# Optimization experiments

Hardware: AMD Instinct MI355X
Metric: run time of the kernel (lower is better)

The kernel has to match this reference:

```python
import jax, jax.numpy as jnp
import numpy as np
import math

IN_DIM = 256
OUT_DIM = 256
H = 4
DK = OUT_DIM // H  # 64
N = 40000
E = 300000
T = 2  # node types
R = 3  # relations: 0:(A->B), 1:(B->A), 2:(A->B)


def setup_inputs() -> dict:
    key = jax.random.key(0)
    ks = jax.random.split(key, 24)
    def xavier(k, shape):
        fan_in, fan_out = shape[-2], shape[-1]
        lim = math.sqrt(6.0 / (fan_in + fan_out))
        return jax.random.uniform(k, shape, jnp.float32, -lim, lim)
    inp = {
        "hA": jax.random.normal(ks[0], (N, IN_DIM), jnp.float32),
        "hB": jax.random.normal(ks[1], (N, IN_DIM), jnp.float32),
        "src0": jax.random.randint(ks[2], (E,), 0, N, jnp.int32),
        "dst0": jax.random.randint(ks[3], (E,), 0, N, jnp.int32),
        "src1": jax.random.randint(ks[4], (E,), 0, N, jnp.int32),
        "dst1": jax.random.randint(ks[5], (E,), 0, N, jnp.int32),
        "src2": jax.random.randint(ks[6], (E,), 0, N, jnp.int32),
        "dst2": jax.random.randint(ks[7], (E,), 0, N, jnp.int32),
        # per-node-type linear weights, stacked [T, in, out]
        "Wk": xavier(ks[8], (T, IN_DIM, OUT_DIM)),
        "bk": jnp.zeros((T, OUT_DIM), jnp.float32),
        "Wq": xavier(ks[9], (T, IN_DIM, OUT_DIM)),
        "bq": jnp.zeros((T, OUT_DIM), jnp.float32),
        "Wv": xavier(ks[10], (T, IN_DIM, OUT_DIM)),
        "bv": jnp.zeros((T, OUT_DIM), jnp.float32),
        "Wa": xavier(ks[11], (T, OUT_DIM, OUT_DIM)),
        "ba": jnp.zeros((T, OUT_DIM), jnp.float32),
        "rel_att": xavier(ks[12], (R, H, DK, DK)),
        "rel_msg": xavier(ks[13], (R, H, DK, DK)),
        "rel_pri": jnp.ones((R, H), jnp.float32),
        "skip": jnp.ones((T,), jnp.float32),
    }
    return inp


def _hgt_forward(hA, hB, Wk, bk, Wq, bq, Wv, bv, Wa, ba,
                 rel_att, rel_msg, rel_pri, skip, edges):
    h = [hA, hB]
    sqrt_dk = math.sqrt(DK)

    def proj(W, b, x, t):
        return (x @ W[t] + b[t]).reshape(-1, H, DK)

    def rel_agg(r, s, d, src, dst):
        # relation-specific transforms
        k = jnp.einsum('nhi,hij->nhj', proj(Wk, bk, h[s], s), rel_att[r])
        v = jnp.einsum('nhi,hij->nhj', proj(Wv, bv, h[s], s), rel_msg[r])
        q = proj(Wq, bq, h[d], d)
        nd = h[d].shape[0]
        # per-edge dot-product attention score [E, H]
        score = jnp.einsum('ehd,ehd->eh', q[dst], k[src]) * rel_pri[r] / sqrt_dk
        # edge softmax normalized by destination node
        m = jax.ops.segment_max(score, dst, num_segments=nd)
        e = jnp.exp(score - m[dst])
        denom = jax.ops.segment_sum(e, dst, num_segments=nd)
        attn = e / denom[dst]
        # weighted scatter-sum aggregation -> [nd, H, DK]
        return jax.ops.segment_sum(v[src] * attn[:, :, None], dst, num_segments=nd)

    (src0, dst0), (src1, dst1), (src2, dst2) = edges
    agg0 = rel_agg(0, 0, 1, src0, dst0)  # A -> B
    agg1 = rel_agg(1, 1, 0, src1, dst1)  # B -> A
    agg2 = rel_agg(2, 0, 1, src2, dst2)  # A -> B

    # cross_reducer='mean' over etypes per destination type
    t_A = agg1.reshape(-1, OUT_DIM)
    t_B = ((agg0 + agg2) * 0.5).reshape(-1, OUT_DIM)

    def ts_aggr(t, n_id, h_dst):
        alpha = jax.nn.sigmoid(skip[n_id])
        trans = t @ Wa[n_id] + ba[n_id]  # dropout p=0.0 -> identity
        return trans * alpha + h_dst * (1.0 - alpha)

    out_A = ts_aggr(t_A, 0, hA)
    out_B = ts_aggr(t_B, 1, hB)
    return jnp.stack([out_A, out_B])  # [2, N, OUT_DIM]


def reference(hA, hB, src0, dst0, src1, dst1, src2, dst2,
              Wk, bk, Wq, bq, Wv, bv, Wa, ba,
              rel_att, rel_msg, rel_pri, skip):
    edges = ((src0, dst0), (src1, dst1), (src2, dst2))
    return _hgt_forward(hA, hB, Wk, bk, Wq, bq, Wv, bv, Wa, ba,
                        rel_att, rel_msg, rel_pri, skip, edges)
```

## Files before the change

kernel.cpp:

```cpp
#include <hip/hip_runtime.h>

#define NN 40000
#define EE 300000
#define DIM 256
#define NHD 4
#define CAP 64
#define LOG2E 1.4426950408889634f

typedef __attribute__((ext_vector_type(8))) short bfrag;
typedef __attribute__((ext_vector_type(4))) float fx4;

static __device__ __forceinline__ float bflo(unsigned u) {
  union { unsigned i; float f; } v; v.i = u << 16; return v.f;
}
static __device__ __forceinline__ float bfhi(unsigned u) {
  union { unsigned i; float f; } v; v.i = u & 0xffff0000u; return v.f;
}
static __device__ __forceinline__ unsigned short f2bf(float f) {
  union { float f; unsigned i; } v; v.f = f;
  unsigned x = v.i;
  return (unsigned short)((x + 0x7fffu + ((x >> 16) & 1u)) >> 16);
}
static __device__ __forceinline__ void gload_lds16(const unsigned short* g, unsigned short* l) {
  __builtin_amdgcn_global_load_lds((const __attribute__((address_space(1))) void*)g,
                                   (__attribute__((address_space(3))) void*)l, 16, 0, 0);
}

static __device__ __forceinline__ void map_rc(int L, int NC, int NR, int& rb, int& cb) {
  int per = 8 * NC;
  int g = L / per;
  int base = g * 8;
  int rig = NR - base; if (rig > 8) rig = 8;
  int idx = L - g * per;
  rb = base + idx % rig;
  cb = idx / rig;
}

static __device__ __forceinline__ void gemm_core64(const unsigned short* __restrict__ X,
                                                   const unsigned short* __restrict__ WT,
                                                   int R0, int C0,
                                                   fx4 acc[2][4],
                                                   unsigned short* ldsA,
                                                   unsigned short* ldsB) {
  const int tid = threadIdx.x;
  const int wave = tid >> 6, lane = tid & 63;
  const int li = lane & 15, lk = lane >> 4;
  const int wr = wave >> 1, wc = wave & 1;
  const int lr = lane >> 3;
  const int swz = ((lane & 7) ^ lr) * 8;
#pragma unroll
  for (int kt = 0; kt < 4; ++kt) {
    const int k0 = kt * 64;
    if (kt) __syncthreads();
#pragma unroll
    for (int i = 0; i < 6; ++i) {
      int g = wave * 6 + i;
      if (g < 8) gload_lds16(X + (size_t)(R0 + g * 8 + lr) * DIM + k0 + swz, ldsA + g * 512);
      else       gload_lds16(WT + (size_t)(C0 + (g - 8) * 8 + lr) * DIM + k0 + swz, ldsB + (g - 8) * 512);
    }
    __syncthreads();
#pragma unroll
    for (int ks = 0; ks < 2; ++ks) {
      bfrag a[2], b[4];
      const int chb = (lk + ks * 4) ^ (li & 7);
#pragma unroll
      for (int mt = 0; mt < 2; ++mt)
        a[mt] = *(const bfrag*)(ldsA + (wr * 32 + mt * 16 + li) * 64 + chb * 8);
#pragma unroll
      for (int nt = 0; nt < 4; ++nt)
        b[nt] = *(const bfrag*)(ldsB + (wc * 64 + nt * 16 + li) * 64 + chb * 8);
#pragma unroll
      for (int mt = 0; mt < 2; ++mt)
#pragma unroll
        for (int nt = 0; nt < 4; ++nt)
          acc[mt][nt] = __builtin_amdgcn_mfma_f32_16x16x32_bf16(a[mt], b[nt], acc[mt][nt], 0, 0, 0);
    }
  }
}

__global__ __launch_bounds__(256) void cvt_kernel(const float* __restrict__ hA,
                                                  const float* __restrict__ hB,
                                                  unsigned short* __restrict__ XA,
                                                  unsigned short* __restrict__ XB) {
  long id = (long)blockIdx.x * 256 + threadIdx.x;
  const long half = (long)NN * DIM / 8;
  const float4* src; unsigned short* dst; long o;
  if (id < half) { src = (const float4*)hA; dst = XA; o = id; }
  else           { src = (const float4*)hB; dst = XB; o = id - half; }
  float4 a = src[o * 2], b = src[o * 2 + 1];
  uint4 pk;
  pk.x = (unsigned)f2bf(a.x) | ((unsigned)f2bf(a.y) << 16);
  pk.y = (unsigned)f2bf(a.z) | ((unsigned)f2bf(a.w) << 16);
  pk.z = (unsigned)f2bf(b.x) | ((unsigned)f2bf(b.y) << 16);
  pk.w = (unsigned)f2bf(b.z) | ((unsigned)f2bf(b.w) << 16);
  ((uint4*)dst)[o] = pk;
}

__global__ __launch_bounds__(256) void prep_weights(
    const float* __restrict__ Wk, const float* __restrict__ bk,
    const float* __restrict__ Wq, const float* __restrict__ bq,
    const float* __restrict__ Wv, const float* __restrict__ bv,
    const float* __restrict__ Wa,
    const float* __restrict__ rel_att, const float* __restrict__ rel_msg,
    const float* __restrict__ rel_pri,
    unsigned short* __restrict__ WT_A, unsigned short* __restrict__ WT_B,
    unsigned short* __restrict__ WaT, float* __restrict__ biasA, float* __restrict__ biasB) {
  int id = blockIdx.x * 256 + threadIdx.x;
  if (id < 262144) {
    int c = id >> 8, i = id & 255;
    int br = c >> 9, w = c & 511, h = w >> 7, ww = w & 127;
    int iskv = (ww >> 2) & 1;
    int j = (ww >> 3) * 4 + (ww & 3);
    int r = br ? 2 : 0;
    const float* W  = iskv ? Wv : Wk;
    const float* RM = iskv ? rel_msg : rel_att;
    const float* wrow = W + i * 256 + h * 64;
    const float* rm = RM + (size_t)((r * NHD + h) * 64) * 64 + j;
    float s = 0.f;
#pragma unroll 8
    for (int l = 0; l < 64; l++) s += wrow[l] * rm[l * 64];
    if (!iskv) s *= rel_pri[r * NHD + h] * 0.125f * LOG2E;
    WT_A[c * 256 + i] = f2bf(s);
    return;
  }
  id -= 262144;
  if (id < 65536) {
    int c = id >> 8, i = id & 255;
    WT_A[(1024 + c) * 256 + i] = f2bf(Wq[i * 256 + c]);
    return;
  }
  id -= 65536;
  if (id < 131072) {
    int c = id >> 8, i = id & 255;
    int h = c >> 7, ww = c & 127;
    int iskv = (ww >> 2) & 1;
    int j = (ww >> 3) * 4 + (ww & 3);
    const float* W  = iskv ? Wv : Wk;
    const float* RM = iskv ? rel_msg : rel_att;
    const float* wrow = W + 65536 + i * 256 + h * 64;
    const float* rm = RM + (size_t)((1 * NHD + h) * 64) * 64 + j;
    float s = 0.f;
#pragma unroll 8
    for (int l = 0; l < 64; l++) s += wrow[l] * rm[l * 64];
    if (!iskv) s *= rel_pri[1 * NHD + h] * 0.125f * LOG2E;
    WT_B[c * 256 + i] = f2bf(s);
    return;
  }
  id -= 131072;
  if (id < 65536) {
    int c = id >> 8, i = id & 255;
    WT_B[(512 + c) * 256 + i] = f2bf(Wq[65536 + i * 256 + c]);
    return;
  }
  id -= 65536;
  if (id < 131072) {
    int t = id >> 16, rem = id & 65535, c = rem >> 8, i = rem & 255;
    WaT[t * 65536 + c * 256 + i] = f2bf(Wa[t * 65536 + i * 256 + c]);
    return;
  }
  id -= 131072;
  if (id < 2048) {
    if (id < 1280) {
      int c = id; float s;
      if (c < 1024) {
        int br = c >> 9, w = c & 511, h = w >> 7, ww = w & 127;
        int iskv = (ww >> 2) & 1;
        int j = (ww >> 3) * 4 + (ww & 3);
        int r = br ? 2 : 0;
        const float* B  = iskv ? bv : bk;
        const float* RM = iskv ? rel_msg : rel_att;
        s = 0.f;
        for (int l = 0; l < 64; l++)
          s += B[h * 64 + l] * RM[(size_t)((r * NHD + h) * 64 + l) * 64 + j];
        if (!iskv) s *= rel_pri[r * NHD + h] * 0.125f * LOG2E;
      } else s = bq[c - 1024];
      biasA[c] = s;
    } else {
      int c = id - 1280; float s;
      if (c < 512) {
        int h = c >> 7, ww = c & 127;
        int iskv = (ww >> 2) & 1;
        int j = (ww >> 3) * 4 + (ww & 3);
        const float* B  = iskv ? bv : bk;
        const float* RM = iskv ? rel_msg : rel_att;
        s = 0.f;
        for (int l = 0; l < 64; l++)
          s += B[256 + h * 64 + l] * RM[(size_t)((1 * NHD + h) * 64 + l) * 64 + j];
        if (!iskv) s *= rel_pri[1 * NHD + h] * 0.125f * LOG2E;
      } else s = bq[256 + (c - 512)];
      biasB[c] = s;
    }
  }
}

__global__ __launch_bounds__(256) void bucket_build(const int* __restrict__ src0, const int* __restrict__ dst0,
                                                    const int* __restrict__ src1, const int* __restrict__ dst1,
                                                    const int* __restrict__ src2, const int* __restrict__ dst2,
                                                    int* __restrict__ cnt, int* __restrict__ bkt) {
  int e = blockIdx.x * 256 + threadIdx.x;
  if (e >= EE) return;
  int r = blockIdx.y;
  const int* src = r == 0 ? src0 : (r == 1 ? src1 : src2);
  const int* dst = r == 0 ? dst0 : (r == 1 ? dst1 : dst2);
  int d = dst[e];
  int pos = atomicAdd(&cnt[r * NN + d], 1);
  if (pos < CAP) bkt[(size_t)r * NN * CAP + d * CAP + pos] = src[e];
}

__global__ __launch_bounds__(256) void gemm_kvq(const unsigned short* __restrict__ X,
                                                const unsigned short* __restrict__ WT,
                                                const float* __restrict__ bias,
                                                unsigned short* __restrict__ Out,
                                                int ldOut, int NC) {
  __shared__ unsigned short ldsA[4096], ldsB[8192];
  fx4 acc[2][4] = {};
  int rb, cb; map_rc(blockIdx.x, NC, 625, rb, cb);
  const int R0 = rb * 64, C0 = cb * 128;
  gemm_core64(X, WT, R0, C0, acc, ldsA, ldsB);
  const int wave = threadIdx.x >> 6, lane = threadIdx.x & 63;
  const int li = lane & 15, lk = lane >> 4;
  const int wr = wave >> 1, wc = wave & 1;
#pragma unroll
  for (int mt = 0; mt < 2; mt++)
#pragma unroll
    for (int nt = 0; nt < 4; nt++) {
      int col = C0 + wc * 64 + nt * 16 + li;
      float bcol = bias[col];
      int rbase = R0 + wr * 32 + mt * 16 + lk * 4;
#pragma unroll
      for (int i = 0; i < 4; i++)
        Out[(long)(rbase + i) * ldOut + col] = f2bf(acc[mt][nt][i] + bcol);
    }
}

template<int LD>
static __device__ __forceinline__ void proc_bucket(const unsigned short* __restrict__ Out,
                                                   int c, int srcs, int kvoff,
                                                   float q0, float q1, float q2, float q3,
                                                   float& L, float& A0, float& A1, float& A2, float& A3) {
  const uint4 Z = {0u, 0u, 0u, 0u};
  auto ldx = [&](int E) -> uint4 {
    int s = __builtin_amdgcn_readlane(srcs, E & 63);
    return *(const uint4*)(Out + (size_t)s * LD + kvoff);
  };
  auto proc = [&](uint4 u) {
    float pp = q0 * bflo(u.x) + q1 * bfhi(u.x) + q2 * bflo(u.y) + q3 * bfhi(u.y);
    pp += __shfl_xor(pp, 1); pp += __shfl_xor(pp, 2);
    pp += __shfl_xor(pp, 4); pp += __shfl_xor(pp, 8);
    float p = exp2f(pp);
    L += p;
    A0 += p * bflo(u.z); A1 += p * bfhi(u.z);
    A2 += p * bflo(u.w); A3 += p * bfhi(u.w);
  };
  uint4 e0 = Z, e1 = Z, e2 = Z, e3 = Z;
  if (0 < c) e0 = ldx(0);
  if (1 < c) e1 = ldx(1);
  if (2 < c) e2 = ldx(2);
  if (3 < c) e3 = ldx(3);
  for (int e = 0; e < c; e += 4) {
    uint4 f0 = Z, f1 = Z, f2 = Z, f3 = Z;
    if (e + 4 < c) f0 = ldx(e + 4);
    if (e + 5 < c) f1 = ldx(e + 5);
    if (e + 6 < c) f2 = ldx(e + 6);
    if (e + 7 < c) f3 = ldx(e + 7);
    proc(e0);
    if (e + 1 < c) proc(e1);
    if (e + 2 < c) proc(e2);
    if (e + 3 < c) proc(e3);
    e0 = f0; e1 = f1; e2 = f2; e3 = f3;
  }
}

__global__ __launch_bounds__(256) void agg_all(const unsigned short* __restrict__ OutA,
                                               const unsigned short* __restrict__ OutB,
                                               const int* __restrict__ cnt,
                                               const int* __restrict__ bkt,
                                               unsigned short* __restrict__ tA,
                                               unsigned short* __restrict__ tB) {
  int wid = (blockIdx.x * 256 + threadIdx.x) >> 6;
  int lane = threadIdx.x & 63;
  int h = lane >> 4, li = lane & 15;
  int qoff = h * 64 + li * 4;
  int kvoff = h * 128 + li * 8;
  if (wid < NN) {
    int n = wid;
    uint2 qr = *(const uint2*)(OutB + (size_t)n * 768 + 512 + qoff);
    float q0 = bflo(qr.x), q1 = bfhi(qr.x), q2 = bflo(qr.y), q3 = bfhi(qr.y);
    int c0 = min(cnt[n], CAP);
    int c2 = min(cnt[2 * NN + n], CAP);
    int s0 = (lane < c0) ? bkt[(size_t)n * CAP + lane] : 0;
    int s2 = (lane < c2) ? bkt[(size_t)2 * NN * CAP + n * CAP + lane] : 0;
    float l0 = 0.f, b00 = 0.f, b01 = 0.f, b02 = 0.f, b03 = 0.f;
    float l2 = 0.f, b20 = 0.f, b21 = 0.f, b22 = 0.f, b23 = 0.f;
    proc_bucket<1280>(OutA,       c0, s0, kvoff, q0, q1, q2, q3, l0, b00, b01, b02, b03);
    proc_bucket<1280>(OutA + 512, c2, s2, kvoff, q0, q1, q2, q3, l2, b20, b21, b22, b23);
    float i0 = (l0 > 0.f) ? 0.5f / l0 : 0.f;
    float i2 = (l2 > 0.f) ? 0.5f / l2 : 0.f;
    float r0 = b00 * i0 + b20 * i2, r1 = b01 * i0 + b21 * i2;
    float r2 = b02 * i0 + b22 * i2, r3 = b03 * i0 + b23 * i2;
    uint2 pk;
    pk.x = (unsigned)f2bf(r0) | ((unsigned)f2bf(r1) << 16);
    pk.y = (unsigned)f2bf(r2) | ((unsigned)f2bf(r3) << 16);
    *(uint2*)(tB + (size_t)n * DIM + qoff) = pk;
  } else if (wid < 2 * NN) {
    int n = wid - NN;
    uint2 qr = *(const uint2*)(OutA + (size_t)n * 1280 + 1024 + qoff);
    float q0 = bflo(qr.x), q1 = bfhi(qr.x), q2 = bflo(qr.y), q3 = bfhi(qr.y);
    int c = min(cnt[NN + n], CAP);
    int s1 = (lane < c) ? bkt[(size_t)NN * CAP + n * CAP + lane] : 0;
    float l = 0.f, a0 = 0.f, a1 = 0.f, a2 = 0.f, a3 = 0.f;
    proc_bucket<768>(OutB, c, s1, kvoff, q0, q1, q2, q3, l, a0, a1, a2, a3);
    float inv = (l > 0.f) ? 1.f / l : 0.f;
    uint2 pk;
    pk.x = (unsigned)f2bf(a0 * inv) | ((unsigned)f2bf(a1 * inv) << 16);
    pk.y = (unsigned)f2bf(a2 * inv) | ((unsigned)f2bf(a3 * inv) << 16);
    *(uint2*)(tA + (size_t)n * DIM + qoff) = pk;
  }
}

__global__ __launch_bounds__(256) void gemm_final2(const unsigned short* __restrict__ tA,
                                                   const unsigned short* __restrict__ tB,
                                                   const unsigned short* __restrict__ XA,
                                                   const unsigned short* __restrict__ XB,
                                                   const unsigned short* __restrict__ WaT,
                                                   const float* __restrict__ ba,
                                                   const float* __restrict__ skip,
                                                   float* __restrict__ outp) {
  __shared__ unsigned short ldsA[4096], ldsB[8192];
  const int t = blockIdx.y;
  const unsigned short* Tt = t ? tB : tA;
  const unsigned short* hin = t ? XB : XA;
  float* op = outp + (size_t)t * NN * DIM;
  fx4 acc[2][4] = {};
  int rb, cb; map_rc(blockIdx.x, 2, 625, rb, cb);
  const int R0 = rb * 64, C0 = cb * 128;
  gemm_core64(Tt, WaT + t * 65536, R0, C0, acc, ldsA, ldsB);
  const int wave = threadIdx.x >> 6, lane = threadIdx.x & 63;
  const int li = lane & 15, lk = lane >> 4;
  const int wr = wave >> 1, wc = wave & 1;
  float alpha = 1.f / (1.f + __expf(-skip[t]));
  float beta = 1.f - alpha;
#pragma unroll
  for (int mt = 0; mt < 2; mt++)
#pragma unroll
    for (int nt = 0; nt < 4; nt++) {
      int col = C0 + wc * 64 + nt * 16 + li;
      float bcol = ba[t * 256 + col];
      int rbase = R0 + wr * 32 + mt * 16 + lk * 4;
#pragma unroll
      for (int i = 0; i < 4; i++) {
        int row = rbase + i;
        float hv = bflo((unsigned)hin[(size_t)row * DIM + col]);
        op[(long)row * DIM + col] = (acc[mt][nt][i] + bcol) * alpha + hv * beta;
      }
    }
}

extern "C" void kernel_launch(void* const* d_in, const int* in_sizes, int n_in,
                              void* d_out, int out_size, void* d_ws, size_t ws_size,
                              hipStream_t stream) {
  const float* hA = (const float*)d_in[0];
  const float* hB = (const float*)d_in[1];
  const int* src0 = (const int*)d_in[2];
  const int* dst0 = (const int*)d_in[3];
  const int* src1 = (const int*)d_in[4];
  const int* dst1 = (const int*)d_in[5];
  const int* src2 = (const int*)d_in[6];
  const int* dst2 = (const int*)d_in[7];
  const float* Wk = (const float*)d_in[8];
  const float* bk = (const float*)d_in[9];
  const float* Wq = (const float*)d_in[10];
  const float* bq = (const float*)d_in[11];
  const float* Wv = (const float*)d_in[12];
  const float* bv = (const float*)d_in[13];
  const float* Wa = (const float*)d_in[14];
  const float* ba = (const float*)d_in[15];
  const float* rel_att = (const float*)d_in[16];
  const float* rel_msg = (const float*)d_in[17];
  const float* rel_pri = (const float*)d_in[18];
  const float* skip = (const float*)d_in[19];

  char* w = (char*)d_ws;
  unsigned short* XA   = (unsigned short*)(w);
  unsigned short* XB   = (unsigned short*)(w + 20480000);
  unsigned short* OutA = (unsigned short*)(w + 40960000);
  unsigned short* OutB = (unsigned short*)(w + 143360000);
  unsigned short* WT_A = (unsigned short*)(w + 204800000);
  unsigned short* WT_B = (unsigned short*)(w + 205455360);
  unsigned short* WaT  = (unsigned short*)(w + 205848576);
  float* biasA = (float*)(w + 206110720);
  float* biasB = (float*)(w + 206115840);
  int* cnt  = (int*)(w + 206118912);
  int* bkt  = (int*)(w + 206598912);
  unsigned short* tA = (unsigned short*)(w + 237318912);
  unsigned short* tB = (unsigned short*)(w + 257798912);

  hipMemsetAsync(cnt, 0, 3 * NN * sizeof(int), stream);
  cvt_kernel<<<10000, 256, 0, stream>>>(hA, hB, XA, XB);
  prep_weights<<<2568, 256, 0, stream>>>(Wk, bk, Wq, bq, Wv, bv, Wa,
                                         rel_att, rel_msg, rel_pri,
                                         WT_A, WT_B, WaT, biasA, biasB);
  bucket_build<<<dim3((EE + 255) / 256, 3), 256, 0, stream>>>(src0, dst0, src1, dst1, src2, dst2, cnt, bkt);
  gemm_kvq<<<6250, 256, 0, stream>>>(XA, WT_A, biasA, OutA, 1280, 10);
  gemm_kvq<<<3750, 256, 0, stream>>>(XB, WT_B, biasB, OutB, 768, 6);
  agg_all<<<20000, 256, 0, stream>>>(OutA, OutB, cnt, bkt, tA, tB);
  gemm_final2<<<dim3(1250, 2), 256, 0, stream>>>(tA, tB, XA, XB, WaT, ba, skip, (float*)d_out);
}
```

Baseline: 358.2 us.

## Fuse fp32-to-bf16 conversion into GEMM load and merge prep kernels

Removes the standalone cvt kernel. The KVQ GEMM now reads fp32 hA/hB directly and converts them to bf16 while staging into swizzled LDS. Bucket building is folded into the weight-prep kernel, and the two KVQ GEMM launches are merged into one grid. The final GEMM reads the fp32 residual directly. This cuts launches and a 40MB write-plus-reread round trip, but the A tile now goes through register loads instead of async global_load_lds and is read at twice the bytes for each column block.

```diff
diff --git a/kernel.cpp b/kernel.cpp
--- a/kernel.cpp
+++ b/kernel.cpp
@@ -8,6 +8,7 @@
 #define LOG2E 1.4426950408889634f
 
 typedef __attribute__((ext_vector_type(8))) short bfrag;
+typedef __attribute__((ext_vector_type(8))) unsigned short ubfrag;
 typedef __attribute__((ext_vector_type(4))) float fx4;
 
 static __device__ __forceinline__ float bflo(unsigned u) {
@@ -36,27 +37,38 @@
   cb = idx / rig;
 }
 
-static __device__ __forceinline__ void gemm_core64(const unsigned short* __restrict__ X,
-                                                   const unsigned short* __restrict__ WT,
-                                                   int R0, int C0,
-                                                   fx4 acc[2][4],
-                                                   unsigned short* ldsA,
-                                                   unsigned short* ldsB) {
+static __device__ __forceinline__ void gemm_core64_f32A(const float* __restrict__ X,
+                                                        const unsigned short* __restrict__ WT,
+                                                        int R0, int C0,
+                                                        fx4 acc[2][4],
+                                                        unsigned short* ldsA,
+                                                        unsigned short* ldsB) {
   const int tid = threadIdx.x;
   const int wave = tid >> 6, lane = tid & 63;
   const int li = lane & 15, lk = lane >> 4;
   const int wr = wave >> 1, wc = wave & 1;
   const int lr = lane >> 3;
   const int swz = ((lane & 7) ^ lr) * 8;
+  const int rowA0 = tid >> 3, chA = tid & 7;
 #pragma unroll
   for (int kt = 0; kt < 4; ++kt) {
     const int k0 = kt * 64;
     if (kt) __syncthreads();
 #pragma unroll
-    for (int i = 0; i < 6; ++i) {
-      int g = wave * 6 + i;
-      if (g < 8) gload_lds16(X + (size_t)(R0 + g * 8 + lr) * DIM + k0 + swz, ldsA + g * 512);
-      else       gload_lds16(WT + (size_t)(C0 + (g - 8) * 8 + lr) * DIM + k0 + swz, ldsB + (g - 8) * 512);
+    for (int i = 0; i < 4; ++i) {
+      int g = wave * 4 + i;
+      gload_lds16(WT + (size_t)(C0 + g * 8 + lr) * DIM + k0 + swz, ldsB + g * 512);
+    }
+#pragma unroll
+    for (int j = 0; j < 2; ++j) {
+      int row = rowA0 + j * 32;
+      const float* s = X + (size_t)(R0 + row) * DIM + k0 + chA * 8;
+      float4 u = *(const float4*)s, v = *(const float4*)(s + 4);
+      ubfrag pk;
+      pk[0] = f2bf(u.x); pk[1] = f2bf(u.y); pk[2] = f2bf(u.z); pk[3] = f2bf(u.w);
+      pk[4] = f2bf(v.x); pk[5] = f2bf(v.y); pk[6] = f2bf(v.z); pk[7] = f2bf(v.w);
+      int sch = chA ^ (row & 7);
+      *(ubfrag*)(ldsA + row * 64 + sch * 8) = pk;
     }
     __syncthreads();
 #pragma unroll
@@ -78,25 +90,7 @@
   }
 }
 
-__global__ __launch_bounds__(256) void cvt_kernel(const float* __restrict__ hA,
-                                                  const float* __restrict__ hB,
-                                                  unsigned short* __restrict__ XA,
-                                                  unsigned short* __restrict__ XB) {
-  long id = (long)blockIdx.x * 256 + threadIdx.x;
-  const long half = (long)NN * DIM / 8;
-  const float4* src; unsigned short* dst; long o;
-  if (id < half) { src = (const float4*)hA; dst = XA; o = id; }
-  else           { src = (const float4*)hB; dst = XB; o = id - half; }
-  float4 a = src[o * 2], b = src[o * 2 + 1];
-  uint4 pk;
-  pk.x = (unsigned)f2bf(a.x) | ((unsigned)f2bf(a.y) << 16);
-  pk.y = (unsigned)f2bf(a.z) | ((unsigned)f2bf(a.w) << 16);
-  pk.z = (unsigned)f2bf(b.x) | ((unsigned)f2bf(b.y) << 16);
-  pk.w = (unsigned)f2bf(b.z) | ((unsigned)f2bf(b.w) << 16);
-  ((uint4*)dst)[o] = pk;
-}
-
-__global__ __launch_bounds__(256) void prep_weights(
+__global__ __launch_bounds__(256) void prep_all(
     const float* __restrict__ Wk, const float* __restrict__ bk,
     const float* __restrict__ Wq, const float* __restrict__ bq,
     const float* __restrict__ Wv, const float* __restrict__ bv,
@@ -104,7 +98,23 @@
     const float* __restrict__ rel_att, const float* __restrict__ rel_msg,
     const float* __restrict__ rel_pri,
     unsigned short* __restrict__ WT_A, unsigned short* __restrict__ WT_B,
-    unsigned short* __restrict__ WaT, float* __restrict__ biasA, float* __restrict__ biasB) {
+    unsigned short* __restrict__ WaT, float* __restrict__ biasA, float* __restrict__ biasB,
+    const int* __restrict__ src0, const int* __restrict__ dst0,
+    const int* __restrict__ src1, const int* __restrict__ dst1,
+    const int* __restrict__ src2, const int* __restrict__ dst2,
+    int* __restrict__ cnt, int* __restrict__ bkt) {
+  if (blockIdx.x >= 2568) {
+    int bb = blockIdx.x - 2568;
+    int r = bb / 1172;
+    int e = (bb % 1172) * 256 + threadIdx.x;
+    if (e >= EE) return;
+    const int* src = r == 0 ? src0 : (r == 1 ? src1 : src2);
+    const int* dst = r == 0 ? dst0 : (r == 1 ? dst1 : dst2);
+    int d = dst[e];
+    int pos = atomicAdd(&cnt[r * NN + d], 1);
+    if (pos < CAP) bkt[(size_t)r * NN * CAP + d * CAP + pos] = src[e];
+    return;
+  }
   int id = blockIdx.x * 256 + threadIdx.x;
   if (id < 262144) {
     int c = id >> 8, i = id & 255;
@@ -193,30 +203,23 @@
   }
 }
 
-__global__ __launch_bounds__(256) void bucket_build(const int* __restrict__ src0, const int* __restrict__ dst0,
-                                                    const int* __restrict__ src1, const int* __restrict__ dst1,
-                                                    const int* __restrict__ src2, const int* __restrict__ dst2,
-                                                    int* __restrict__ cnt, int* __restrict__ bkt) {
-  int e = blockIdx.x * 256 + threadIdx.x;
-  if (e >= EE) return;
-  int r = blockIdx.y;
-  const int* src = r == 0 ? src0 : (r == 1 ? src1 : src2);
-  const int* dst = r == 0 ? dst0 : (r == 1 ? dst1 : dst2);
-  int d = dst[e];
-  int pos = atomicAdd(&cnt[r * NN + d], 1);
-  if (pos < CAP) bkt[(size_t)r * NN * CAP + d * CAP + pos] = src[e];
-}
-
-__global__ __launch_bounds__(256) void gemm_kvq(const unsigned short* __restrict__ X,
-                                                const unsigned short* __restrict__ WT,
-                                                const float* __restrict__ bias,
-                                                unsigned short* __restrict__ Out,
-                                                int ldOut, int NC) {
+__global__ __launch_bounds__(256) void gemm_kvq(const float* __restrict__ hA,
+                                                const float* __restrict__ hB,
+                                                const unsigned short* __restrict__ WT_A,
+                                                const unsigned short* __restrict__ WT_B,
+                                                const float* __restrict__ biasA,
+                                                const float* __restrict__ biasB,
+                                                unsigned short* __restrict__ OutA,
+                                                unsigned short* __restrict__ OutB) {
   __shared__ unsigned short ldsA[4096], ldsB[8192];
+  const float* X; const unsigned short* WT; const float* bias;
+  unsigned short* Out; int ldOut, NC, Lb;
+  if (blockIdx.x < 6250) { X = hA; WT = WT_A; bias = biasA; Out = OutA; ldOut = 1280; NC = 10; Lb = blockIdx.x; }
+  else                   { X = hB; WT = WT_B; bias = biasB; Out = OutB; ldOut = 768;  NC = 6;  Lb = blockIdx.x - 6250; }
   fx4 acc[2][4] = {};
-  int rb, cb; map_rc(blockIdx.x, NC, 625, rb, cb);
+  int rb, cb; map_rc(Lb, NC, 625, rb, cb);
   const int R0 = rb * 64, C0 = cb * 128;
-  gemm_core64(X, WT, R0, C0, acc, ldsA, ldsB);
+  gemm_core64_f32A(X, WT, R0, C0, acc, ldsA, ldsB);
   const int wave = threadIdx.x >> 6, lane = threadIdx.x & 63;
   const int li = lane & 15, lk = lane >> 4;
   const int wr = wave >> 1, wc = wave & 1;
@@ -318,10 +321,52 @@
   }
 }
 
+static __device__ __forceinline__ void gemm_core64_bf16A(const unsigned short* __restrict__ X,
+                                                         const unsigned short* __restrict__ WT,
+                                                         int R0, int C0,
+                                                         fx4 acc[2][4],
+                                                         unsigned short* ldsA,
+                                                         unsigned short* ldsB) {
+  const int tid = threadIdx.x;
+  const int wave = tid >> 6, lane = tid & 63;
+  const int li = lane & 15, lk = lane >> 4;
+  const int wr = wave >> 1, wc = wave & 1;
+  const int lr = lane >> 3;
+  const int swz = ((lane & 7) ^ lr) * 8;
+#pragma unroll
+  for (int kt = 0; kt < 4; ++kt) {
+    const int k0 = kt * 64;
+    if (kt) __syncthreads();
+#pragma unroll
+    for (int i = 0; i < 6; ++i) {
+      int g = wave * 6 + i;
+      if (g < 8) gload_lds16(X + (size_t)(R0 + g * 8 + lr) * DIM + k0 + swz, ldsA + g * 512);
+      else       gload_lds16(WT + (size_t)(C0 + (g - 8) * 8 + lr) * DIM + k0 + swz, ldsB + (g - 8) * 512);
+    }
+    __syncthreads();
+#pragma unroll
+    for (int ks = 0; ks < 2; ++ks) {
+      bfrag a[2], b[4];
+      const int chb = (lk + ks * 4) ^ (li & 7);
+#pragma unroll
+      for (int mt = 0; mt < 2; ++mt)
+        a[mt] = *(const bfrag*)(ldsA + (wr * 32 + mt * 16 + li) * 64 + chb * 8);
+#pragma unroll
+      for (int nt = 0; nt < 4; ++nt)
+        b[nt] = *(const bfrag*)(ldsB + (wc * 64 + nt * 16 + li) * 64 + chb * 8);
+#pragma unroll
+      for (int mt = 0; mt < 2; ++mt)
+#pragma unroll
+        for (int nt = 0; nt < 4; ++nt)
+          acc[mt][nt] = __builtin_amdgcn_mfma_f32_16x16x32_bf16(a[mt], b[nt], acc[mt][nt], 0, 0, 0);
+    }
+  }
+}
+
 __global__ __launch_bounds__(256) void gemm_final2(const unsigned short* __restrict__ tA,
                                                    const unsigned short* __restrict__ tB,
-                                                   const unsigned short* __restrict__ XA,
-                                                   const unsigned short* __restrict__ XB,
+                                                   const float* __restrict__ hA,
+                                                   const float* __restrict__ hB,
                                                    const unsigned short* __restrict__ WaT,
                                                    const float* __restrict__ ba,
                                                    const float* __restrict__ skip,
@@ -329,12 +374,12 @@
   __shared__ unsigned short ldsA[4096], ldsB[8192];
   const int t = blockIdx.y;
   const unsigned short* Tt = t ? tB : tA;
-  const unsigned short* hin = t ? XB : XA;
+  const float* hin = t ? hB : hA;
   float* op = outp + (size_t)t * NN * DIM;
   fx4 acc[2][4] = {};
   int rb, cb; map_rc(blockIdx.x, 2, 625, rb, cb);
   const int R0 = rb * 64, C0 = cb * 128;
-  gemm_core64(Tt, WaT + t * 65536, R0, C0, acc, ldsA, ldsB);
+  gemm_core64_bf16A(Tt, WaT + t * 65536, R0, C0, acc, ldsA, ldsB);
   const int wave = threadIdx.x >> 6, lane = threadIdx.x & 63;
   const int li = lane & 15, lk = lane >> 4;
   const int wr = wave >> 1, wc = wave & 1;
@@ -350,7 +395,7 @@
 #pragma unroll
       for (int i = 0; i < 4; i++) {
         int row = rbase + i;
-        float hv = bflo((unsigned)hin[(size_t)row * DIM + col]);
+        float hv = hin[(size_t)row * DIM + col];
         op[(long)row * DIM + col] = (acc[mt][nt][i] + bcol) * alpha + hv * beta;
       }
     }
@@ -381,8 +426,6 @@
   const float* skip = (const float*)d_in[19];
 
   char* w = (char*)d_ws;
-  unsigned short* XA   = (unsigned short*)(w);
-  unsigned short* XB   = (unsigned short*)(w + 20480000);
   unsigned short* OutA = (unsigned short*)(w + 40960000);
   unsigned short* OutB = (unsigned short*)(w + 143360000);
   unsigned short* WT_A = (unsigned short*)(w + 204800000);
@@ -396,13 +439,11 @@
   unsigned short* tB = (unsigned short*)(w + 257798912);
 
   hipMemsetAsync(cnt, 0, 3 * NN * sizeof(int), stream);
-  cvt_kernel<<<10000, 256, 0, stream>>>(hA, hB, XA, XB);
-  prep_weights<<<2568, 256, 0, stream>>>(Wk, bk, Wq, bq, Wv, bv, Wa,
-                                         rel_att, rel_msg, rel_pri,
-                                         WT_A, WT_B, WaT, biasA, biasB);
-  bucket_build<<<dim3((EE + 255) / 256, 3), 256, 0, stream>>>(src0, dst0, src1, dst1, src2, dst2, cnt, bkt);
-  gemm_kvq<<<6250, 256, 0, stream>>>(XA, WT_A, biasA, OutA, 1280, 10);
-  gemm_kvq<<<3750, 256, 0, stream>>>(XB, WT_B, biasB, OutB, 768, 6);
+  prep_all<<<6084, 256, 0, stream>>>(Wk, bk, Wq, bq, Wv, bv, Wa,
+                                     rel_att, rel_msg, rel_pri,
+                                     WT_A, WT_B, WaT, biasA, biasB,
+                                     src0, dst0, src1, dst1, src2, dst2, cnt, bkt);
+  gemm_kvq<<<10000, 256, 0, stream>>>(hA, hB, WT_A, WT_B, biasA, biasB, OutA, OutB);
   agg_all<<<20000, 256, 0, stream>>>(OutA, OutB, cnt, bkt, tA, tB);
-  gemm_final2<<<dim3(1250, 2), 256, 0, stream>>>(tA, tB, XA, XB, WaT, ba, skip, (float*)d_out);
-}
+  gemm_final2<<<dim3(1250, 2), 256, 0, stream>>>(tA, tB, hA, hB, WaT, ba, skip, (float*)d_out);
+}
```

Measured after the change: 381.8 us. +6.6%, slower.

## Enlarge GEMM row tile to 128 and fuse edge bucketing into weight prep

Applied to the files above, without the earlier changes.

The shared GEMM core now computes 128x128 output tiles instead of 64x128, so each wave holds a 4x4 accumulator grid. This reuses each loaded weight tile across twice as many rows and halves the block count for the projection and output GEMMs. Rows past the end of the matrix are clamped on load and masked on store. Separately, the edge bucket-building kernel is merged into the weight preparation kernel as extra blocks, removing one launch and letting the two run concurrently. The larger tile raises register and LDS use per block, which may lower occupancy.

```diff
diff --git a/kernel.cpp b/kernel.cpp
--- a/kernel.cpp
+++ b/kernel.cpp
@@ -36,12 +36,12 @@
   cb = idx / rig;
 }
 
-static __device__ __forceinline__ void gemm_core64(const unsigned short* __restrict__ X,
-                                                   const unsigned short* __restrict__ WT,
-                                                   int R0, int C0,
-                                                   fx4 acc[2][4],
-                                                   unsigned short* ldsA,
-                                                   unsigned short* ldsB) {
+static __device__ __forceinline__ void gemm_core128(const unsigned short* __restrict__ X,
+                                                    const unsigned short* __restrict__ WT,
+                                                    int R0, int C0,
+                                                    fx4 acc[4][4],
+                                                    unsigned short* ldsA,
+                                                    unsigned short* ldsB) {
   const int tid = threadIdx.x;
   const int wave = tid >> 6, lane = tid & 63;
   const int li = lane & 15, lk = lane >> 4;
@@ -53,24 +53,28 @@
     const int k0 = kt * 64;
     if (kt) __syncthreads();
 #pragma unroll
-    for (int i = 0; i < 6; ++i) {
-      int g = wave * 6 + i;
-      if (g < 8) gload_lds16(X + (size_t)(R0 + g * 8 + lr) * DIM + k0 + swz, ldsA + g * 512);
-      else       gload_lds16(WT + (size_t)(C0 + (g - 8) * 8 + lr) * DIM + k0 + swz, ldsB + (g - 8) * 512);
+    for (int i = 0; i < 8; ++i) {
+      int g = wave * 8 + i;
+      if (g < 16) {
+        int ra = min(R0 + g * 8 + lr, NN - 1);
+        gload_lds16(X + (size_t)ra * DIM + k0 + swz, ldsA + g * 512);
+      } else {
+        gload_lds16(WT + (size_t)(C0 + (g - 16) * 8 + lr) * DIM + k0 + swz, ldsB + (g - 16) * 512);
+      }
     }
     __syncthreads();
 #pragma unroll
     for (int ks = 0; ks < 2; ++ks) {
-      bfrag a[2], b[4];
+      bfrag a[4], b[4];
       const int chb = (lk + ks * 4) ^ (li & 7);
 #pragma unroll
-      for (int mt = 0; mt < 2; ++mt)
-        a[mt] = *(const bfrag*)(ldsA + (wr * 32 + mt * 16 + li) * 64 + chb * 8);
+      for (int mt = 0; mt < 4; ++mt)
+        a[mt] = *(const bfrag*)(ldsA + (wr * 64 + mt * 16 + li) * 64 + chb * 8);
 #pragma unroll
       for (int nt = 0; nt < 4; ++nt)
         b[nt] = *(const bfrag*)(ldsB + (wc * 64 + nt * 16 + li) * 64 + chb * 8);
 #pragma unroll
-      for (int mt = 0; mt < 2; ++mt)
+      for (int mt = 0; mt < 4; ++mt)
 #pragma unroll
         for (int nt = 0; nt < 4; ++nt)
           acc[mt][nt] = __builtin_amdgcn_mfma_f32_16x16x32_bf16(a[mt], b[nt], acc[mt][nt], 0, 0, 0);
@@ -96,7 +100,7 @@
   ((uint4*)dst)[o] = pk;
 }
 
-__global__ __launch_bounds__(256) void prep_weights(
+__global__ __launch_bounds__(256) void prep_all(
     const float* __restrict__ Wk, const float* __restrict__ bk,
     const float* __restrict__ Wq, const float* __restrict__ bq,
     const float* __restrict__ Wv, const float* __restrict__ bv,
@@ -104,7 +108,23 @@
     const float* __restrict__ rel_att, const float* __restrict__ rel_msg,
     const float* __restrict__ rel_pri,
     unsigned short* __restrict__ WT_A, unsigned short* __restrict__ WT_B,
-    unsigned short* __restrict__ WaT, float* __restrict__ biasA, float* __restrict__ biasB) {
+    unsigned short* __restrict__ WaT, float* __restrict__ biasA, float* __restrict__ biasB,
+    const int* __restrict__ src0, const int* __restrict__ dst0,
+    const int* __restrict__ src1, const int* __restrict__ dst1,
+    const int* __restrict__ src2, const int* __restrict__ dst2,
+    int* __restrict__ cnt, int* __restrict__ bkt) {
+  if (blockIdx.x >= 2568) {
+    int bb = blockIdx.x - 2568;
+    int r = bb / 1172;
+    int e = (bb % 1172) * 256 + threadIdx.x;
+    if (e >= EE) return;
+    const int* src = r == 0 ? src0 : (r == 1 ? src1 : src2);
+    const int* dst = r == 0 ? dst0 : (r == 1 ? dst1 : dst2);
+    int d = dst[e];
+    int pos = atomicAdd(&cnt[r * NN + d], 1);
+    if (pos < CAP) bkt[(size_t)r * NN * CAP + d * CAP + pos] = src[e];
+    return;
+  }
   int id = blockIdx.x * 256 + threadIdx.x;
   if (id < 262144) {
     int c = id >> 8, i = id & 255;
@@ -193,43 +213,31 @@
   }
 }
 
-__global__ __launch_bounds__(256) void bucket_build(const int* __restrict__ src0, const int* __restrict__ dst0,
-                                                    const int* __restrict__ src1, const int* __restrict__ dst1,
-                                                    const int* __restrict__ src2, const int* __restrict__ dst2,
-                                                    int* __restrict__ cnt, int* __restrict__ bkt) {
-  int e = blockIdx.x * 256 + threadIdx.x;
-  if (e >= EE) return;
-  int r = blockIdx.y;
-  const int* src = r == 0 ? src0 : (r == 1 ? src1 : src2);
-  const int* dst = r == 0 ? dst0 : (r == 1 ? dst1 : dst2);
-  int d = dst[e];
-  int pos = atomicAdd(&cnt[r * NN + d], 1);
-  if (pos < CAP) bkt[(size_t)r * NN * CAP + d * CAP + pos] = src[e];
-}
-
 __global__ __launch_bounds__(256) void gemm_kvq(const unsigned short* __restrict__ X,
                                                 const unsigned short* __restrict__ WT,
                                                 const float* __restrict__ bias,
                                                 unsigned short* __restrict__ Out,
                                                 int ldOut, int NC) {
-  __shared__ unsigned short ldsA[4096], ldsB[8192];
-  fx4 acc[2][4] = {};
-  int rb, cb; map_rc(blockIdx.x, NC, 625, rb, cb);
-  const int R0 = rb * 64, C0 = cb * 128;
-  gemm_core64(X, WT, R0, C0, acc, ldsA, ldsB);
+  __shared__ unsigned short ldsA[8192], ldsB[8192];
+  fx4 acc[4][4] = {};
+  int rb, cb; map_rc(blockIdx.x, NC, 313, rb, cb);
+  const int R0 = rb * 128, C0 = cb * 128;
+  gemm_core128(X, WT, R0, C0, acc, ldsA, ldsB);
   const int wave = threadIdx.x >> 6, lane = threadIdx.x & 63;
   const int li = lane & 15, lk = lane >> 4;
   const int wr = wave >> 1, wc = wave & 1;
 #pragma unroll
-  for (int mt = 0; mt < 2; mt++)
+  for (int mt = 0; mt < 4; mt++)
 #pragma unroll
     for (int nt = 0; nt < 4; nt++) {
       int col = C0 + wc * 64 + nt * 16 + li;
       float bcol = bias[col];
-      int rbase = R0 + wr * 32 + mt * 16 + lk * 4;
-#pragma unroll
-      for (int i = 0; i < 4; i++)
-        Out[(long)(rbase + i) * ldOut + col] = f2bf(acc[mt][nt][i] + bcol);
+      int rbase = R0 + wr * 64 + mt * 16 + lk * 4;
+#pragma unroll
+      for (int i = 0; i < 4; i++) {
+        int row = rbase + i;
+        if (row < NN) Out[(long)row * ldOut + col] = f2bf(acc[mt][nt][i] + bcol);
+      }
     }
 }
 
@@ -326,32 +334,34 @@
                                                    const float* __restrict__ ba,
                                                    const float* __restrict__ skip,
                                                    float* __restrict__ outp) {
-  __shared__ unsigned short ldsA[4096], ldsB[8192];
+  __shared__ unsigned short ldsA[8192], ldsB[8192];
   const int t = blockIdx.y;
   const unsigned short* Tt = t ? tB : tA;
   const unsigned short* hin = t ? XB : XA;
   float* op = outp + (size_t)t * NN * DIM;
-  fx4 acc[2][4] = {};
-  int rb, cb; map_rc(blockIdx.x, 2, 625, rb, cb);
-  const int R0 = rb * 64, C0 = cb * 128;
-  gemm_core64(Tt, WaT + t * 65536, R0, C0, acc, ldsA, ldsB);
+  fx4 acc[4][4] = {};
+  int rb, cb; map_rc(blockIdx.x, 2, 313, rb, cb);
+  const int R0 = rb * 128, C0 = cb * 128;
+  gemm_core128(Tt, WaT + t * 65536, R0, C0, acc, ldsA, ldsB);
   const int wave = threadIdx.x >> 6, lane = threadIdx.x & 63;
   const int li = lane & 15, lk = lane >> 4;
   const int wr = wave >> 1, wc = wave & 1;
   float alpha = 1.f / (1.f + __expf(-skip[t]));
   float beta = 1.f - alpha;
 #pragma unroll
-  for (int mt = 0; mt < 2; mt++)
+  for (int mt = 0; mt < 4; mt++)
 #pragma unroll
     for (int nt = 0; nt < 4; nt++) {
       int col = C0 + wc * 64 + nt * 16 + li;
       float bcol = ba[t * 256 + col];
-      int rbase = R0 + wr * 32 + mt * 16 + lk * 4;
+      int rbase = R0 + wr * 64 + mt * 16 + lk * 4;
 #pragma unroll
       for (int i = 0; i < 4; i++) {
         int row = rbase + i;
-        float hv = bflo((unsigned)hin[(size_t)row * DIM + col]);
-        op[(long)row * DIM + col] = (acc[mt][nt][i] + bcol) * alpha + hv * beta;
+        if (row < NN) {
+          float hv = bflo((unsigned)hin[(size_t)row * DIM + col]);
+          op[(long)row * DIM + col] = (acc[mt][nt][i] + bcol) * alpha + hv * beta;
+        }
       }
     }
 }
@@ -397,12 +407,12 @@
 
   hipMemsetAsync(cnt, 0, 3 * NN * sizeof(int), stream);
   cvt_kernel<<<10000, 256, 0, stream>>>(hA, hB, XA, XB);
-  prep_weights<<<2568, 256, 0, stream>>>(Wk, bk, Wq, bq, Wv, bv, Wa,
-                                         rel_att, rel_msg, rel_pri,
-                                         WT_A, WT_B, WaT, biasA, biasB);
-  bucket_build<<<dim3((EE + 255) / 256, 3), 256, 0, stream>>>(src0, dst0, src1, dst1, src2, dst2, cnt, bkt);
-  gemm_kvq<<<6250, 256, 0, stream>>>(XA, WT_A, biasA, OutA, 1280, 10);
-  gemm_kvq<<<3750, 256, 0, stream>>>(XB, WT_B, biasB, OutB, 768, 6);
+  prep_all<<<6084, 256, 0, stream>>>(Wk, bk, Wq, bq, Wv, bv, Wa,
+                                     rel_att, rel_msg, rel_pri,
+                                     WT_A, WT_B, WaT, biasA, biasB,
+                                     src0, dst0, src1, dst1, src2, dst2, cnt, bkt);
+  gemm_kvq<<<3130, 256, 0, stream>>>(XA, WT_A, biasA, OutA, 1280, 10);
+  gemm_kvq<<<1878, 256, 0, stream>>>(XB, WT_B, biasB, OutB, 768, 6);
   agg_all<<<20000, 256, 0, stream>>>(OutA, OutB, cnt, bkt, tA, tB);
-  gemm_final2<<<dim3(1250, 2), 256, 0, stream>>>(tA, tB, XA, XB, WaT, ba, skip, (float*)d_out);
-}
+  gemm_final2<<<dim3(626, 2), 256, 0, stream>>>(tA, tB, XA, XB, WaT, ba, skip, (float*)d_out);
+}
```

Result: slower. 419.8 us (+17.2%).
